# Performance work log

Measured on AMD Instinct MI355X. Metric: run time of the kernel, lower is better.

Reference implementation:

```python
import jax, jax.numpy as jnp
import numpy as np

NUP, NDOWN = 15, 15
NELEC = NUP + NDOWN
NATOMS = 10
NDIM = 3
NBATCH = 512
FEAT = 64   # hidden feature dim
K_RBF = 64  # gaussian RBF expansion size
NLAYERS = 2
RBF_CUT = 8.0


def _build_graphs():
    # elec-elec: upper-tri pairs, each pair -> 2 directed edges (i->j, j->i),
    # matching ree.repeat_interleave(2) edge-distance ordering.
    ii, jj = np.triu_indices(NELEC, k=1)                      # [435]
    ee_src = np.stack([ii, jj], 1).reshape(-1).astype(np.int32)  # [870]
    ee_dst = np.stack([jj, ii], 1).reshape(-1).astype(np.int32)
    ee_types = np.array([0] * NUP + [1] * NDOWN, np.int32)
    # elec-nuc: nodes = [electrons(0..29), atoms(30..39)];
    # ren is transposed to [natoms, nelec] then flattened -> atom-major pair order.
    aa = np.repeat(np.arange(NATOMS), NELEC)
    ee_ = np.tile(np.arange(NELEC), NATOMS)
    en_src = np.stack([ee_, NELEC + aa], 1).reshape(-1).astype(np.int32)  # [600]
    en_dst = np.stack([NELEC + aa, ee_], 1).reshape(-1).astype(np.int32)
    en_types = np.concatenate([np.array([0] * NUP + [1] * NDOWN),
                               2 + np.arange(NATOMS)]).astype(np.int32)
    return ee_src, ee_dst, ee_types, en_src, en_dst, en_types


def setup_inputs() -> dict:
    key = jax.random.key(0)
    ks = jax.random.split(key, 20)
    ee_src, ee_dst, ee_types, en_src, en_dst, en_types = _build_graphs()
    s = 0.1
    inp = {
        "pos": jax.random.normal(ks[0], (NBATCH, NELEC * NDIM), jnp.float32) * 2.0,
        "atoms": jax.random.normal(ks[1], (NATOMS, NDIM), jnp.float32) * 3.0,
        "emb_ee": jax.random.normal(ks[2], (2, FEAT), jnp.float32) * s,
        "wf_ee": jax.random.normal(ks[3], (K_RBF, FEAT), jnp.float32) * s,
        "bf_ee": jnp.zeros((FEAT,), jnp.float32),
        "wl_ee": jax.random.normal(ks[4], (NLAYERS, FEAT, FEAT), jnp.float32) * s,
        "bl_ee": jnp.zeros((NLAYERS, FEAT), jnp.float32),
        "wr_ee": jax.random.normal(ks[5], (FEAT, 1), jnp.float32) * s,
        "br_ee": jnp.zeros((1,), jnp.float32),
        "emb_en": jax.random.normal(ks[6], (2 + NATOMS, FEAT), jnp.float32) * s,
        "wf_en": jax.random.normal(ks[7], (K_RBF, FEAT), jnp.float32) * s,
        "bf_en": jnp.zeros((FEAT,), jnp.float32),
        "wl_en": jax.random.normal(ks[8], (NLAYERS, FEAT, FEAT), jnp.float32) * s,
        "bl_en": jnp.zeros((NLAYERS, FEAT), jnp.float32),
        "wr_en": jax.random.normal(ks[9], (FEAT, 1), jnp.float32) * s,
        "br_en": jnp.zeros((1,), jnp.float32),
        "ee_src": jnp.asarray(ee_src), "ee_dst": jnp.asarray(ee_dst),
        "ee_types": jnp.asarray(ee_types),
        "en_src": jnp.asarray(en_src), "en_dst": jnp.asarray(en_dst),
        "en_types": jnp.asarray(en_types),
    }
    return inp


def _gnn_kernel(types, src, dst, edist, emb, wf, bf, wl, bl, wr, br):
    """MGCN-style interaction net on a batch of identical graphs.
    types [N] int, src/dst [E] int, edist [nb, E] float."""
    nb = edist.shape[0]
    N = types.shape[0]
    centers = jnp.linspace(0.0, RBF_CUT, K_RBF).astype(edist.dtype)
    rbf = jnp.exp(-(edist[..., None] - centers) ** 2)        # [nb, E, K]
    filt = jnp.tanh(rbf @ wf + bf)                           # [nb, E, F]
    h = jnp.broadcast_to(emb[types][None], (nb, N, emb.shape[1]))  # [nb, N, F]
    for l in range(wl.shape[0]):
        m = h[:, src, :] * filt                              # gather + edge filter
        agg = jnp.zeros_like(h).at[:, dst, :].add(m)         # scatter-add messages
        h = h + jnp.tanh(agg @ wl[l] + bl[l])
    return h.sum(axis=1) @ wr + br                           # [nb, 1] readout


def reference(pos, atoms, emb_ee, wf_ee, bf_ee, wl_ee, bl_ee, wr_ee, br_ee,
              emb_en, wf_en, bf_en, wl_en, bl_en, wr_en, br_en,
              ee_src, ee_dst, ee_types, en_src, en_dst, en_types):
    nb = pos.shape[0]
    xyz = pos.reshape(nb, NELEC, NDIM)
    # elec-elec edge distances (src/dst index electron nodes; symmetric so this
    # equals extract_tri_up(...).repeat_interleave(2))
    d_ee = jnp.linalg.norm(xyz[:, ee_src] - xyz[:, ee_dst], axis=-1)   # [nb, 870]
    # elec-nuc: node positions = [electrons; atoms]
    nodepos = jnp.concatenate(
        [xyz, jnp.broadcast_to(atoms[None], (nb, NATOMS, NDIM))], axis=1)
    d_en = jnp.linalg.norm(nodepos[:, en_src] - nodepos[:, en_dst], axis=-1)  # [nb, 600]
    ee_k = _gnn_kernel(ee_types, ee_src, ee_dst, d_ee,
                       emb_ee, wf_ee, bf_ee, wl_ee, bl_ee, wr_ee, br_ee)
    en_k = _gnn_kernel(en_types, en_src, en_dst, d_en,
                       emb_en, wf_en, bf_en, wl_en, bl_en, wr_en, br_en)
    return jnp.exp(ee_k + en_k)   # [nb, 1] Jastrow factor (derivative=0)
```

## Files before the change

kernel.cpp:

```cpp
#include <hip/hip_runtime.h>
#include <math.h>

#define NB      512
#define NELEC   30
#define NATOMS  10
#define NNEN    40
#define FEAT    64
#define KRBF    64
#define BLOCK   1024
#define NWAVES  (BLOCK/64)
#define NPEE    435
#define NPEN    300
#define TILE    32
#define FPAD    65

#define OFF_XYZ    0
#define OFF_AXYZ   96
#define OFF_KEE    128
#define OFF_BASE   132
#define HS_OFF     OFF_BASE
#define AGG_OFF    (HS_OFF + NNEN*FEAT)
#define FILT_OFF   (AGG_OFF + NNEN*FEAT)
#define SM_TOTAL   (FILT_OFF + NPEE*FPAD)

__device__ __forceinline__ int ee_base(int i) { return 29*i - ((i*(i-1))>>1); }

__global__ __launch_bounds__(BLOCK)
void fused_kernel(const float* __restrict__ pos,
                  const float* __restrict__ atoms,
                  const float* __restrict__ emb_ee,
                  const float* __restrict__ wf_ee,
                  const float* __restrict__ bf_ee,
                  const float* __restrict__ wl_ee,
                  const float* __restrict__ bl_ee,
                  const float* __restrict__ wr_ee,
                  const float* __restrict__ br_ee,
                  const float* __restrict__ emb_en,
                  const float* __restrict__ wf_en,
                  const float* __restrict__ bf_en,
                  const float* __restrict__ wl_en,
                  const float* __restrict__ bl_en,
                  const float* __restrict__ wr_en,
                  const float* __restrict__ br_en,
                  const int*   __restrict__ ee_ty,
                  const int*   __restrict__ en_ty,
                  float*       __restrict__ out)
{
    extern __shared__ float sm[];
    float*  xyz  = sm + OFF_XYZ;
    float*  axyz = sm + OFF_AXYZ;
    double* keeP = reinterpret_cast<double*>(sm + OFF_KEE);
    float*  hS   = sm + HS_OFF;
    float*  aggS = sm + AGG_OFF;
    float*  filt = sm + FILT_OFF;

    const int tid  = threadIdx.x;
    const int b    = blockIdx.x;
    const int lane = tid & 63;
    const int w    = tid >> 6;
    const int q    = tid & 511;
    const int uoff = __builtin_amdgcn_readfirstlane((tid >> 9) * TILE);

    for (int idx = tid; idx < NELEC*3; idx += BLOCK) xyz[idx] = pos[b*NELEC*3 + idx];
    for (int idx = tid; idx < NATOMS*3; idx += BLOCK) axyz[idx] = atoms[idx];
    for (int idx = tid; idx < NELEC*FEAT; idx += BLOCK) {
        int n = idx >> 6, f = idx & 63;
        hS[idx] = emb_ee[ee_ty[n]*FEAT + f];
    }
    __syncthreads();

    {
        const int p = (q < NPEE) ? q : (NPEE - 1);
        {
            int i = 0, rem = p;
            while (rem >= NELEC - 1 - i) { rem -= NELEC - 1 - i; ++i; }
            const int j = i + 1 + rem;
            const float dx = xyz[3*i+0] - xyz[3*j+0];
            const float dy = xyz[3*i+1] - xyz[3*j+1];
            const float dz = xyz[3*i+2] - xyz[3*j+2];
            const float dd = sqrtf(dx*dx + dy*dy + dz*dz);

            float facc[TILE];
            const float* bfH = bf_ee + uoff;
            #pragma unroll
            for (int f = 0; f < TILE; ++f) facc[f] = bfH[f];
            #pragma unroll 2
            for (int k = 0; k < KRBF; ++k) {
                const float ck = (float)((double)k * (8.0/63.0));
                const float t  = dd - ck;
                const float rk = expf(-t*t);
                const float* wrow = wf_ee + k*FEAT + uoff;
                #pragma unroll
                for (int f = 0; f < TILE; ++f) facc[f] = fmaf(rk, wrow[f], facc[f]);
            }
            #pragma unroll
            for (int ff = 0; ff < TILE; ++ff)
                filt[p*FPAD + uoff + ff] = tanhf(facc[ff]);
        }
        __syncthreads();

        #pragma unroll
        for (int l = 0; l < 2; ++l) {
            const float* wlL = wl_ee + l*FEAT*FEAT;
            const float* blL = bl_ee + l*FEAT;

            #pragma unroll
            for (int pass = 0; pass < 2; ++pass) {
                const int idx = tid + pass*BLOCK;
                if (idx < NELEC*FEAT) {
                    const int i = idx >> 6;
                    const int f = idx & 63;
                    float a = 0.f;
                    #pragma unroll
                    for (int j = 0; j < NELEC; ++j) {
                        if (j != i) {
                            int pp = (j < i) ? (ee_base(j) + (i - j - 1))
                                             : (ee_base(i) + (j - i - 1));
                            a = fmaf(hS[j*FEAT + f], filt[pp*FPAD + f], a);
                        }
                    }
                    aggS[i*FEAT + f] = a;
                }
            }
            __syncthreads();

            for (int i = w; i < NELEC; i += NWAVES) {
                float a2 = 0.f;
                const float4* arow = reinterpret_cast<const float4*>(aggS + i*FEAT);
                #pragma unroll
                for (int k = 0; k < FEAT/4; ++k) {
                    float4 av = arow[k];
                    a2 = fmaf(av.x, wlL[(4*k+0)*FEAT + lane], a2);
                    a2 = fmaf(av.y, wlL[(4*k+1)*FEAT + lane], a2);
                    a2 = fmaf(av.z, wlL[(4*k+2)*FEAT + lane], a2);
                    a2 = fmaf(av.w, wlL[(4*k+3)*FEAT + lane], a2);
                }
                hS[i*FEAT + lane] += tanhf(a2 + blL[lane]);
            }
            __syncthreads();
        }

        if (w == 0) {
            float s = 0.f;
            #pragma unroll
            for (int n = 0; n < NELEC; ++n) s += hS[n*FEAT + lane];
            double dv = (double)s * (double)wr_ee[lane];
            #pragma unroll
            for (int o = 32; o > 0; o >>= 1) dv += __shfl_xor(dv, o, 64);
            if (lane == 0) *keeP = dv + (double)br_ee[0];
        }
    }
    __syncthreads();

    {
        for (int idx = tid; idx < NNEN*FEAT; idx += BLOCK) {
            int n = idx >> 6, f = idx & 63;
            hS[idx] = emb_en[en_ty[n]*FEAT + f];
        }

        const int p = (q < NPEN) ? q : (NPEN - 1);
        {
            const int a = p / NELEC;
            const int e = p - a*NELEC;
            const float dx = xyz[3*e+0] - axyz[3*a+0];
            const float dy = xyz[3*e+1] - axyz[3*a+1];
            const float dz = xyz[3*e+2] - axyz[3*a+2];
            const float dd = sqrtf(dx*dx + dy*dy + dz*dz);

            float facc[TILE];
            const float* bfH = bf_en + uoff;
            #pragma unroll
            for (int f = 0; f < TILE; ++f) facc[f] = bfH[f];
            #pragma unroll 2
            for (int k = 0; k < KRBF; ++k) {
                const float ck = (float)((double)k * (8.0/63.0));
                const float t  = dd - ck;
                const float rk = expf(-t*t);
                const float* wrow = wf_en + k*FEAT + uoff;
                #pragma unroll
                for (int f = 0; f < TILE; ++f) facc[f] = fmaf(rk, wrow[f], facc[f]);
            }
            #pragma unroll
            for (int ff = 0; ff < TILE; ++ff)
                filt[p*FPAD + uoff + ff] = tanhf(facc[ff]);
        }
        __syncthreads();

        #pragma unroll
        for (int l = 0; l < 2; ++l) {
            const float* wlL = wl_en + l*FEAT*FEAT;
            const float* blL = bl_en + l*FEAT;

            #pragma unroll
            for (int pass = 0; pass < 3; ++pass) {
                const int idx = tid + pass*BLOCK;
                if (idx < NNEN*FEAT) {
                    const int n = idx >> 6;
                    const int f = idx & 63;
                    float a = 0.f;
                    if (n < NELEC) {
                        #pragma unroll
                        for (int at = 0; at < NATOMS; ++at)
                            a = fmaf(hS[(NELEC+at)*FEAT + f],
                                     filt[(at*NELEC + n)*FPAD + f], a);
                    } else {
                        const int at = n - NELEC;
                        #pragma unroll
                        for (int e2 = 0; e2 < NELEC; ++e2)
                            a = fmaf(hS[e2*FEAT + f],
                                     filt[(at*NELEC + e2)*FPAD + f], a);
                    }
                    aggS[n*FEAT + f] = a;
                }
            }
            __syncthreads();

            for (int n = w; n < NNEN; n += NWAVES) {
                float a2 = 0.f;
                const float4* arow = reinterpret_cast<const float4*>(aggS + n*FEAT);
                #pragma unroll
                for (int k = 0; k < FEAT/4; ++k) {
                    float4 av = arow[k];
                    a2 = fmaf(av.x, wlL[(4*k+0)*FEAT + lane], a2);
                    a2 = fmaf(av.y, wlL[(4*k+1)*FEAT + lane], a2);
                    a2 = fmaf(av.z, wlL[(4*k+2)*FEAT + lane], a2);
                    a2 = fmaf(av.w, wlL[(4*k+3)*FEAT + lane], a2);
                }
                hS[n*FEAT + lane] += tanhf(a2 + blL[lane]);
            }
            __syncthreads();
        }

        if (w == 0) {
            float s = 0.f;
            #pragma unroll
            for (int n = 0; n < NNEN; ++n) s += hS[n*FEAT + lane];
            double dv = (double)s * (double)wr_en[lane];
            #pragma unroll
            for (int o = 32; o > 0; o >>= 1) dv += __shfl_xor(dv, o, 64);
            if (lane == 0) out[b] = (float)exp(dv + (double)br_en[0] + *keeP);
        }
    }
}

extern "C" void kernel_launch(void* const* d_in, const int* in_sizes, int n_in,
                              void* d_out, int out_size, void* d_ws, size_t ws_size,
                              hipStream_t stream) {
    const float* pos    = (const float*)d_in[0];
    const float* atoms  = (const float*)d_in[1];
    const float* emb_ee = (const float*)d_in[2];
    const float* wf_ee  = (const float*)d_in[3];
    const float* bf_ee  = (const float*)d_in[4];
    const float* wl_ee  = (const float*)d_in[5];
    const float* bl_ee  = (const float*)d_in[6];
    const float* wr_ee  = (const float*)d_in[7];
    const float* br_ee  = (const float*)d_in[8];
    const float* emb_en = (const float*)d_in[9];
    const float* wf_en  = (const float*)d_in[10];
    const float* bf_en  = (const float*)d_in[11];
    const float* wl_en  = (const float*)d_in[12];
    const float* bl_en  = (const float*)d_in[13];
    const float* wr_en  = (const float*)d_in[14];
    const float* br_en  = (const float*)d_in[15];
    const int*   ee_ty  = (const int*)d_in[18];
    const int*   en_ty  = (const int*)d_in[21];

    float* out = (float*)d_out;

    (void)hipFuncSetAttribute((const void*)fused_kernel,
            hipFuncAttributeMaxDynamicSharedMemorySize, SM_TOTAL*(int)sizeof(float));

    fused_kernel<<<NB, BLOCK, SM_TOTAL*sizeof(float), stream>>>(
        pos, atoms,
        emb_ee, wf_ee, bf_ee, wl_ee, bl_ee, wr_ee, br_ee,
        emb_en, wf_en, bf_en, wl_en, bl_en, wr_en, br_en,
        ee_ty, en_ty, out);
}
```

Before: 221.5 us.

## Fuse aggregation and linear per wave with ping-pong node buffers, fewer barriers

The message aggregation and the dense layer are merged into one per-wave pass. Each wave computes the aggregated row for one node into a private scratch row in shared memory, then applies the weight matrix directly. Node features now alternate between two buffers, so one barrier per layer disappears and the in-place update is gone. The ee readout is overlapped with the en filter computation, and the en filter is split across specific waves with inactive padded threads skipped. The catch is that only 30-40 nodes are processed by 16 waves, so per-layer parallelism drops from one thread per (node, feature) to one wave per node.

```diff
diff --git a/kernel.cpp b/kernel.cpp
--- a/kernel.cpp
+++ b/kernel.cpp
@@ -13,17 +13,109 @@
 #define NPEN    300
 #define TILE    32
 #define FPAD    65
+#define WROW    64
 
 #define OFF_XYZ    0
 #define OFF_AXYZ   96
 #define OFF_KEE    128
-#define OFF_BASE   132
-#define HS_OFF     OFF_BASE
-#define AGG_OFF    (HS_OFF + NNEN*FEAT)
-#define FILT_OFF   (AGG_OFF + NNEN*FEAT)
+#define H0_OFF     132
+#define H1_OFF     (H0_OFF + NNEN*FEAT)
+#define WR_OFF     (H1_OFF + NNEN*FEAT)
+#define FILT_OFF   (WR_OFF + NWAVES*WROW)
 #define SM_TOTAL   (FILT_OFF + NPEE*FPAD)
 
 __device__ __forceinline__ int ee_base(int i) { return 29*i - ((i*(i-1))>>1); }
+
+__device__ __forceinline__ void ee_layer(const float* __restrict__ hc,
+                                         float* __restrict__ hn,
+                                         const float* __restrict__ filt,
+                                         float* __restrict__ wr,
+                                         const float* __restrict__ wlL,
+                                         const float* __restrict__ blL,
+                                         int w, int lane)
+{
+    for (int i = w; i < NELEC; i += NWAVES) {
+        float a = 0.f;
+        #pragma unroll
+        for (int j = 0; j < NELEC; ++j) {
+            if (j != i) {
+                int pp = (j < i) ? (ee_base(j) + (i - j - 1))
+                                 : (ee_base(i) + (j - i - 1));
+                a = fmaf(hc[j*FEAT + lane], filt[pp*FPAD + lane], a);
+            }
+        }
+        wr[lane] = a;
+        float a2 = 0.f;
+        const float4* arow = reinterpret_cast<const float4*>(wr);
+        #pragma unroll
+        for (int k = 0; k < FEAT/4; ++k) {
+            float4 av = arow[k];
+            a2 = fmaf(av.x, wlL[(4*k+0)*FEAT + lane], a2);
+            a2 = fmaf(av.y, wlL[(4*k+1)*FEAT + lane], a2);
+            a2 = fmaf(av.z, wlL[(4*k+2)*FEAT + lane], a2);
+            a2 = fmaf(av.w, wlL[(4*k+3)*FEAT + lane], a2);
+        }
+        hn[i*FEAT + lane] = hc[i*FEAT + lane] + tanhf(a2 + blL[lane]);
+    }
+}
+
+__device__ __forceinline__ void en_layer(const float* __restrict__ hc,
+                                         float* __restrict__ hn,
+                                         const float* __restrict__ filt,
+                                         float* __restrict__ wr,
+                                         const float* __restrict__ wlL,
+                                         const float* __restrict__ blL,
+                                         int w, int lane)
+{
+    for (int n = w; n < NNEN; n += NWAVES) {
+        float a = 0.f;
+        if (n < NELEC) {
+            #pragma unroll
+            for (int at = 0; at < NATOMS; ++at)
+                a = fmaf(hc[(NELEC+at)*FEAT + lane],
+                         filt[(at*NELEC + n)*FPAD + lane], a);
+        } else {
+            const int at = n - NELEC;
+            #pragma unroll
+            for (int e2 = 0; e2 < NELEC; ++e2)
+                a = fmaf(hc[e2*FEAT + lane],
+                         filt[(at*NELEC + e2)*FPAD + lane], a);
+        }
+        wr[lane] = a;
+        float a2 = 0.f;
+        const float4* arow = reinterpret_cast<const float4*>(wr);
+        #pragma unroll
+        for (int k = 0; k < FEAT/4; ++k) {
+            float4 av = arow[k];
+            a2 = fmaf(av.x, wlL[(4*k+0)*FEAT + lane], a2);
+            a2 = fmaf(av.y, wlL[(4*k+1)*FEAT + lane], a2);
+            a2 = fmaf(av.z, wlL[(4*k+2)*FEAT + lane], a2);
+            a2 = fmaf(av.w, wlL[(4*k+3)*FEAT + lane], a2);
+        }
+        hn[n*FEAT + lane] = hc[n*FEAT + lane] + tanhf(a2 + blL[lane]);
+    }
+}
+
+__device__ __forceinline__ void rbf_filter(float dd, const float* __restrict__ wf,
+                                           const float* __restrict__ bf,
+                                           int uoff, float* __restrict__ dstrow)
+{
+    float facc[TILE];
+    const float* bfH = bf + uoff;
+    #pragma unroll
+    for (int f = 0; f < TILE; ++f) facc[f] = bfH[f];
+    #pragma unroll 2
+    for (int k = 0; k < KRBF; ++k) {
+        const float ck = (float)((double)k * (8.0/63.0));
+        const float t  = dd - ck;
+        const float rk = expf(-t*t);
+        const float* wrow = wf + k*FEAT + uoff;
+        #pragma unroll
+        for (int f = 0; f < TILE; ++f) facc[f] = fmaf(rk, wrow[f], facc[f]);
+    }
+    #pragma unroll
+    for (int ff = 0; ff < TILE; ++ff) dstrow[uoff + ff] = tanhf(facc[ff]);
+}
 
 __global__ __launch_bounds__(BLOCK)
 void fused_kernel(const float* __restrict__ pos,
@@ -50,8 +142,9 @@
     float*  xyz  = sm + OFF_XYZ;
     float*  axyz = sm + OFF_AXYZ;
     double* keeP = reinterpret_cast<double*>(sm + OFF_KEE);
-    float*  hS   = sm + HS_OFF;
-    float*  aggS = sm + AGG_OFF;
+    float*  h0   = sm + H0_OFF;
+    float*  h1   = sm + H1_OFF;
+    float*  wrS  = sm + WR_OFF;
     float*  filt = sm + FILT_OFF;
 
     const int tid  = threadIdx.x;
@@ -60,186 +153,80 @@
     const int w    = tid >> 6;
     const int q    = tid & 511;
     const int uoff = __builtin_amdgcn_readfirstlane((tid >> 9) * TILE);
+    float* wr = wrS + w*WROW;
 
     for (int idx = tid; idx < NELEC*3; idx += BLOCK) xyz[idx] = pos[b*NELEC*3 + idx];
     for (int idx = tid; idx < NATOMS*3; idx += BLOCK) axyz[idx] = atoms[idx];
     for (int idx = tid; idx < NELEC*FEAT; idx += BLOCK) {
         int n = idx >> 6, f = idx & 63;
-        hS[idx] = emb_ee[ee_ty[n]*FEAT + f];
-    }
-    __syncthreads();
-
+        h0[idx] = emb_ee[ee_ty[n]*FEAT + f];
+    }
+    __syncthreads();
+
+    if (q < NPEE) {
+        const int p = q;
+        int i = 0, rem = p;
+        while (rem >= NELEC - 1 - i) { rem -= NELEC - 1 - i; ++i; }
+        const int j = i + 1 + rem;
+        const float dx = xyz[3*i+0] - xyz[3*j+0];
+        const float dy = xyz[3*i+1] - xyz[3*j+1];
+        const float dz = xyz[3*i+2] - xyz[3*j+2];
+        const float dd = sqrtf(dx*dx + dy*dy + dz*dz);
+        rbf_filter(dd, wf_ee, bf_ee, uoff, filt + p*FPAD);
+    }
+    __syncthreads();
+
+    ee_layer(h0, h1, filt, wr, wl_ee + 0*FEAT*FEAT, bl_ee + 0*FEAT, w, lane);
+    __syncthreads();
+    ee_layer(h1, h0, filt, wr, wl_ee + 1*FEAT*FEAT, bl_ee + 1*FEAT, w, lane);
+    __syncthreads();
+
+    for (int idx = tid; idx < NNEN*FEAT; idx += BLOCK) {
+        int n = idx >> 6, f = idx & 63;
+        h1[idx] = emb_en[en_ty[n]*FEAT + f];
+    }
     {
-        const int p = (q < NPEE) ? q : (NPEE - 1);
-        {
-            int i = 0, rem = p;
-            while (rem >= NELEC - 1 - i) { rem -= NELEC - 1 - i; ++i; }
-            const int j = i + 1 + rem;
-            const float dx = xyz[3*i+0] - xyz[3*j+0];
-            const float dy = xyz[3*i+1] - xyz[3*j+1];
-            const float dz = xyz[3*i+2] - xyz[3*j+2];
-            const float dd = sqrtf(dx*dx + dy*dy + dz*dz);
-
-            float facc[TILE];
-            const float* bfH = bf_ee + uoff;
-            #pragma unroll
-            for (int f = 0; f < TILE; ++f) facc[f] = bfH[f];
-            #pragma unroll 2
-            for (int k = 0; k < KRBF; ++k) {
-                const float ck = (float)((double)k * (8.0/63.0));
-                const float t  = dd - ck;
-                const float rk = expf(-t*t);
-                const float* wrow = wf_ee + k*FEAT + uoff;
-                #pragma unroll
-                for (int f = 0; f < TILE; ++f) facc[f] = fmaf(rk, wrow[f], facc[f]);
+        const int v = w & 7;
+        const int blk = (w < 8) ? (v < 5 ? v : -1)
+                                : ((v >= 1 && v <= 3) ? v - 1
+                                   : (v == 5 || v == 6) ? v - 2 : -1);
+        if (blk >= 0) {
+            const int p = blk*64 + lane;
+            if (p < NPEN) {
+                const int a = p / NELEC;
+                const int e = p - a*NELEC;
+                const float dx = xyz[3*e+0] - axyz[3*a+0];
+                const float dy = xyz[3*e+1] - axyz[3*a+1];
+                const float dz = xyz[3*e+2] - axyz[3*a+2];
+                const float dd = sqrtf(dx*dx + dy*dy + dz*dz);
+                rbf_filter(dd, wf_en, bf_en, uoff, filt + p*FPAD);
             }
-            #pragma unroll
-            for (int ff = 0; ff < TILE; ++ff)
-                filt[p*FPAD + uoff + ff] = tanhf(facc[ff]);
-        }
-        __syncthreads();
-
-        #pragma unroll
-        for (int l = 0; l < 2; ++l) {
-            const float* wlL = wl_ee + l*FEAT*FEAT;
-            const float* blL = bl_ee + l*FEAT;
-
-            #pragma unroll
-            for (int pass = 0; pass < 2; ++pass) {
-                const int idx = tid + pass*BLOCK;
-                if (idx < NELEC*FEAT) {
-                    const int i = idx >> 6;
-                    const int f = idx & 63;
-                    float a = 0.f;
-                    #pragma unroll
-                    for (int j = 0; j < NELEC; ++j) {
-                        if (j != i) {
-                            int pp = (j < i) ? (ee_base(j) + (i - j - 1))
-                                             : (ee_base(i) + (j - i - 1));
-                            a = fmaf(hS[j*FEAT + f], filt[pp*FPAD + f], a);
-                        }
-                    }
-                    aggS[i*FEAT + f] = a;
-                }
-            }
-            __syncthreads();
-
-            for (int i = w; i < NELEC; i += NWAVES) {
-                float a2 = 0.f;
-                const float4* arow = reinterpret_cast<const float4*>(aggS + i*FEAT);
-                #pragma unroll
-                for (int k = 0; k < FEAT/4; ++k) {
-                    float4 av = arow[k];
-                    a2 = fmaf(av.x, wlL[(4*k+0)*FEAT + lane], a2);
-                    a2 = fmaf(av.y, wlL[(4*k+1)*FEAT + lane], a2);
-                    a2 = fmaf(av.z, wlL[(4*k+2)*FEAT + lane], a2);
-                    a2 = fmaf(av.w, wlL[(4*k+3)*FEAT + lane], a2);
-                }
-                hS[i*FEAT + lane] += tanhf(a2 + blL[lane]);
-            }
-            __syncthreads();
-        }
-
-        if (w == 0) {
-            float s = 0.f;
-            #pragma unroll
-            for (int n = 0; n < NELEC; ++n) s += hS[n*FEAT + lane];
-            double dv = (double)s * (double)wr_ee[lane];
-            #pragma unroll
-            for (int o = 32; o > 0; o >>= 1) dv += __shfl_xor(dv, o, 64);
-            if (lane == 0) *keeP = dv + (double)br_ee[0];
-        }
-    }
-    __syncthreads();
-
-    {
-        for (int idx = tid; idx < NNEN*FEAT; idx += BLOCK) {
-            int n = idx >> 6, f = idx & 63;
-            hS[idx] = emb_en[en_ty[n]*FEAT + f];
-        }
-
-        const int p = (q < NPEN) ? q : (NPEN - 1);
-        {
-            const int a = p / NELEC;
-            const int e = p - a*NELEC;
-            const float dx = xyz[3*e+0] - axyz[3*a+0];
-            const float dy = xyz[3*e+1] - axyz[3*a+1];
-            const float dz = xyz[3*e+2] - axyz[3*a+2];
-            const float dd = sqrtf(dx*dx + dy*dy + dz*dz);
-
-            float facc[TILE];
-            const float* bfH = bf_en + uoff;
-            #pragma unroll
-            for (int f = 0; f < TILE; ++f) facc[f] = bfH[f];
-            #pragma unroll 2
-            for (int k = 0; k < KRBF; ++k) {
-                const float ck = (float)((double)k * (8.0/63.0));
-                const float t  = dd - ck;
-                const float rk = expf(-t*t);
-                const float* wrow = wf_en + k*FEAT + uoff;
-                #pragma unroll
-                for (int f = 0; f < TILE; ++f) facc[f] = fmaf(rk, wrow[f], facc[f]);
-            }
-            #pragma unroll
-            for (int ff = 0; ff < TILE; ++ff)
-                filt[p*FPAD + uoff + ff] = tanhf(facc[ff]);
-        }
-        __syncthreads();
-
-        #pragma unroll
-        for (int l = 0; l < 2; ++l) {
-            const float* wlL = wl_en + l*FEAT*FEAT;
-            const float* blL = bl_en + l*FEAT;
-
-            #pragma unroll
-            for (int pass = 0; pass < 3; ++pass) {
-                const int idx = tid + pass*BLOCK;
-                if (idx < NNEN*FEAT) {
-                    const int n = idx >> 6;
-                    const int f = idx & 63;
-                    float a = 0.f;
-                    if (n < NELEC) {
-                        #pragma unroll
-                        for (int at = 0; at < NATOMS; ++at)
-                            a = fmaf(hS[(NELEC+at)*FEAT + f],
-                                     filt[(at*NELEC + n)*FPAD + f], a);
-                    } else {
-                        const int at = n - NELEC;
-                        #pragma unroll
-                        for (int e2 = 0; e2 < NELEC; ++e2)
-                            a = fmaf(hS[e2*FEAT + f],
-                                     filt[(at*NELEC + e2)*FPAD + f], a);
-                    }
-                    aggS[n*FEAT + f] = a;
-                }
-            }
-            __syncthreads();
-
-            for (int n = w; n < NNEN; n += NWAVES) {
-                float a2 = 0.f;
-                const float4* arow = reinterpret_cast<const float4*>(aggS + n*FEAT);
-                #pragma unroll
-                for (int k = 0; k < FEAT/4; ++k) {
-                    float4 av = arow[k];
-                    a2 = fmaf(av.x, wlL[(4*k+0)*FEAT + lane], a2);
-                    a2 = fmaf(av.y, wlL[(4*k+1)*FEAT + lane], a2);
-                    a2 = fmaf(av.z, wlL[(4*k+2)*FEAT + lane], a2);
-                    a2 = fmaf(av.w, wlL[(4*k+3)*FEAT + lane], a2);
-                }
-                hS[n*FEAT + lane] += tanhf(a2 + blL[lane]);
-            }
-            __syncthreads();
-        }
-
-        if (w == 0) {
-            float s = 0.f;
-            #pragma unroll
-            for (int n = 0; n < NNEN; ++n) s += hS[n*FEAT + lane];
-            double dv = (double)s * (double)wr_en[lane];
-            #pragma unroll
-            for (int o = 32; o > 0; o >>= 1) dv += __shfl_xor(dv, o, 64);
-            if (lane == 0) out[b] = (float)exp(dv + (double)br_en[0] + *keeP);
-        }
+        }
+    }
+    if (w == 0) {
+        float s = 0.f;
+        #pragma unroll
+        for (int n = 0; n < NELEC; ++n) s += h0[n*FEAT + lane];
+        double dv = (double)s * (double)wr_ee[lane];
+        #pragma unroll
+        for (int o = 32; o > 0; o >>= 1) dv += __shfl_xor(dv, o, 64);
+        if (lane == 0) *keeP = dv + (double)br_ee[0];
+    }
+    __syncthreads();
+
+    en_layer(h1, h0, filt, wr, wl_en + 0*FEAT*FEAT, bl_en + 0*FEAT, w, lane);
+    __syncthreads();
+    en_layer(h0, h1, filt, wr, wl_en + 1*FEAT*FEAT, bl_en + 1*FEAT, w, lane);
+    __syncthreads();
+
+    if (w == 0) {
+        float s = 0.f;
+        #pragma unroll
+        for (int n = 0; n < NNEN; ++n) s += h1[n*FEAT + lane];
+        double dv = (double)s * (double)wr_en[lane];
+        #pragma unroll
+        for (int o = 32; o > 0; o >>= 1) dv += __shfl_xor(dv, o, 64);
+        if (lane == 0) out[b] = (float)exp(dv + (double)br_en[0] + *keeP);
     }
 }
 
```

New measurement: 215.8 us. 1.03x faster.

## Keep RBF filter halves in registers and stage them through a half-width LDS buffer

Applied to the files above, without the earlier changes.

Each thread now computes a full pair's filter for one 32-feature half and keeps the tanh outputs in registers. Only one half at a time is written to a 33-float-padded shared buffer, and the aggregation runs in two half passes with the second half written between them. This shrinks shared memory by about half, which may allow more blocks per CU. It also skips the clamped duplicate pair work and swaps the h/agg buffers in the electron-nuclear stage to overlap embedding init with filter compute. The cost is extra barriers, re-writing the filter each layer, and high register pressure from the live facc array.

```diff
diff --git a/kernel.cpp b/kernel.cpp
--- a/kernel.cpp
+++ b/kernel.cpp
@@ -12,18 +12,65 @@
 #define NPEE    435
 #define NPEN    300
 #define TILE    32
-#define FPAD    65
-
-#define OFF_XYZ    0
-#define OFF_AXYZ   96
-#define OFF_KEE    128
-#define OFF_BASE   132
-#define HS_OFF     OFF_BASE
-#define AGG_OFF    (HS_OFF + NNEN*FEAT)
-#define FILT_OFF   (AGG_OFF + NNEN*FEAT)
-#define SM_TOTAL   (FILT_OFF + NPEE*FPAD)
+#define FPAD    33
+
+#define OFF_XYZ   0
+#define OFF_AXYZ  96
+#define OFF_KEE   128
+#define HS_OFF    132
+#define AGG_OFF   (HS_OFF + NNEN*FEAT)
+#define FT_OFF    (AGG_OFF + NNEN*FEAT)
+#define SM_TOTAL  (FT_OFF + NPEE*FPAD)
 
 __device__ __forceinline__ int ee_base(int i) { return 29*i - ((i*(i-1))>>1); }
+
+__device__ __forceinline__ void rbf_filter(float dd, const float* __restrict__ wf,
+                                           const float* __restrict__ bf,
+                                           int uoff, float* __restrict__ facc)
+{
+    const float* bfH = bf + uoff;
+    #pragma unroll
+    for (int f = 0; f < TILE; ++f) facc[f] = bfH[f];
+    #pragma unroll 2
+    for (int k = 0; k < KRBF; ++k) {
+        const float ck = (float)((double)k * (8.0/63.0));
+        const float t  = dd - ck;
+        const float rk = expf(-t*t);
+        const float* wrow = wf + k*FEAT + uoff;
+        #pragma unroll
+        for (int f = 0; f < TILE; ++f) facc[f] = fmaf(rk, wrow[f], facc[f]);
+    }
+    #pragma unroll
+    for (int f = 0; f < TILE; ++f) facc[f] = tanhf(facc[f]);
+}
+
+__device__ __forceinline__ void ft_write(const float* __restrict__ facc,
+                                         float* __restrict__ fT, int p)
+{
+    #pragma unroll
+    for (int ff = 0; ff < TILE; ++ff) fT[p*FPAD + ff] = facc[ff];
+}
+
+__device__ __forceinline__ void dense_update(const float* __restrict__ aggbuf,
+                                             float* __restrict__ hbuf,
+                                             const float* __restrict__ wlL,
+                                             const float* __restrict__ blL,
+                                             int N, int w, int lane)
+{
+    for (int i = w; i < N; i += NWAVES) {
+        float a2 = 0.f;
+        const float4* arow = reinterpret_cast<const float4*>(aggbuf + i*FEAT);
+        #pragma unroll
+        for (int k = 0; k < FEAT/4; ++k) {
+            float4 av = arow[k];
+            a2 = fmaf(av.x, wlL[(4*k+0)*FEAT + lane], a2);
+            a2 = fmaf(av.y, wlL[(4*k+1)*FEAT + lane], a2);
+            a2 = fmaf(av.z, wlL[(4*k+2)*FEAT + lane], a2);
+            a2 = fmaf(av.w, wlL[(4*k+3)*FEAT + lane], a2);
+        }
+        hbuf[i*FEAT + lane] += tanhf(a2 + blL[lane]);
+    }
+}
 
 __global__ __launch_bounds__(BLOCK)
 void fused_kernel(const float* __restrict__ pos,
@@ -52,14 +99,30 @@
     double* keeP = reinterpret_cast<double*>(sm + OFF_KEE);
     float*  hS   = sm + HS_OFF;
     float*  aggS = sm + AGG_OFF;
-    float*  filt = sm + FILT_OFF;
+    float*  fT   = sm + FT_OFF;
 
     const int tid  = threadIdx.x;
     const int b    = blockIdx.x;
     const int lane = tid & 63;
     const int w    = tid >> 6;
-    const int q    = tid & 511;
-    const int uoff = __builtin_amdgcn_readfirstlane((tid >> 9) * TILE);
+
+    const int  ee_t   = (w >= 7) ? 1 : 0;
+    const int  ee_p   = ((w >= 7 ? w - 7 : w) << 6) | lane;
+    const bool ee_ok  = (w < 14) && (ee_p < NPEE);
+    const int  v      = w & 7;
+    const int  en_blk = (w < 8) ? (v < 5 ? v : -1)
+                                : ((v >= 1 && v <= 3) ? v - 1
+                                   : (v == 5 || v == 6) ? v - 2 : -1);
+    const int  en_t   = (w >= 8) ? 1 : 0;
+    const int  en_p   = (en_blk < 0) ? 0 : ((en_blk << 6) | lane);
+    const bool en_ok  = (en_blk >= 0) && (en_p < NPEN);
+    const int  hr     = (w == 5) ? 0 : (w == 6) ? 1 : (w == 7) ? 2
+                      : (w == 8) ? 3 : (w == 12) ? 4 : -1;
+
+    const int uoff_ee = __builtin_amdgcn_readfirstlane(ee_t * TILE);
+    const int uoff_en = __builtin_amdgcn_readfirstlane(en_t * TILE);
+
+    float facc[TILE];
 
     for (int idx = tid; idx < NELEC*3; idx += BLOCK) xyz[idx] = pos[b*NELEC*3 + idx];
     for (int idx = tid; idx < NATOMS*3; idx += BLOCK) axyz[idx] = atoms[idx];
@@ -69,177 +132,129 @@
     }
     __syncthreads();
 
-    {
-        const int p = (q < NPEE) ? q : (NPEE - 1);
-        {
-            int i = 0, rem = p;
-            while (rem >= NELEC - 1 - i) { rem -= NELEC - 1 - i; ++i; }
-            const int j = i + 1 + rem;
-            const float dx = xyz[3*i+0] - xyz[3*j+0];
-            const float dy = xyz[3*i+1] - xyz[3*j+1];
-            const float dz = xyz[3*i+2] - xyz[3*j+2];
-            const float dd = sqrtf(dx*dx + dy*dy + dz*dz);
-
-            float facc[TILE];
-            const float* bfH = bf_ee + uoff;
-            #pragma unroll
-            for (int f = 0; f < TILE; ++f) facc[f] = bfH[f];
-            #pragma unroll 2
-            for (int k = 0; k < KRBF; ++k) {
-                const float ck = (float)((double)k * (8.0/63.0));
-                const float t  = dd - ck;
-                const float rk = expf(-t*t);
-                const float* wrow = wf_ee + k*FEAT + uoff;
+    if (ee_ok) {
+        int i = 0, rem = ee_p;
+        while (rem >= NELEC - 1 - i) { rem -= NELEC - 1 - i; ++i; }
+        const int j = i + 1 + rem;
+        const float dx = xyz[3*i+0] - xyz[3*j+0];
+        const float dy = xyz[3*i+1] - xyz[3*j+1];
+        const float dz = xyz[3*i+2] - xyz[3*j+2];
+        const float dd = sqrtf(dx*dx + dy*dy + dz*dz);
+        rbf_filter(dd, wf_ee, bf_ee, uoff_ee, facc);
+        if (ee_t == 0) ft_write(facc, fT, ee_p);
+    }
+    __syncthreads();
+
+    #pragma unroll
+    for (int l = 0; l < 2; ++l) {
+        const float* wlL = wl_ee + l*FEAT*FEAT;
+        const float* blL = bl_ee + l*FEAT;
+
+        #pragma unroll
+        for (int t = 0; t < 2; ++t) {
+            if (t == 1) {
+                if (ee_ok && ee_t == 1) ft_write(facc, fT, ee_p);
+                __syncthreads();
+            }
+            if (tid < NELEC*TILE) {
+                const int i  = tid >> 5;
+                const int ff = tid & 31;
+                const int f  = t*TILE + ff;
+                float a = 0.f;
                 #pragma unroll
-                for (int f = 0; f < TILE; ++f) facc[f] = fmaf(rk, wrow[f], facc[f]);
-            }
-            #pragma unroll
-            for (int ff = 0; ff < TILE; ++ff)
-                filt[p*FPAD + uoff + ff] = tanhf(facc[ff]);
-        }
+                for (int j = 0; j < NELEC; ++j) {
+                    if (j != i) {
+                        int pp = (j < i) ? (ee_base(j) + (i - j - 1))
+                                         : (ee_base(i) + (j - i - 1));
+                        a = fmaf(hS[j*FEAT + f], fT[pp*FPAD + ff], a);
+                    }
+                }
+                aggS[i*FEAT + f] = a;
+            }
+            __syncthreads();
+        }
+        dense_update(aggS, hS, wlL, blL, NELEC, w, lane);
+        if (l == 0 && ee_ok && ee_t == 0) ft_write(facc, fT, ee_p);
         __syncthreads();
-
-        #pragma unroll
-        for (int l = 0; l < 2; ++l) {
-            const float* wlL = wl_ee + l*FEAT*FEAT;
-            const float* blL = bl_ee + l*FEAT;
-
+    }
+
+    if (w == 15) {
+        float s = 0.f;
+        #pragma unroll
+        for (int n = 0; n < NELEC; ++n) s += hS[n*FEAT + lane];
+        double dv = (double)s * (double)wr_ee[lane];
+        #pragma unroll
+        for (int o = 32; o > 0; o >>= 1) dv += __shfl_xor(dv, o, 64);
+        if (lane == 0) *keeP = dv + (double)br_ee[0];
+    }
+    if (hr >= 0) {
+        #pragma unroll
+        for (int r = 0; r < 8; ++r) {
+            const int idx = hr*64 + lane + r*320;
+            aggS[idx] = emb_en[en_ty[idx >> 6]*FEAT + (idx & 63)];
+        }
+    }
+    if (en_ok) {
+        const int a = en_p / NELEC;
+        const int e = en_p - a*NELEC;
+        const float dx = xyz[3*e+0] - axyz[3*a+0];
+        const float dy = xyz[3*e+1] - axyz[3*a+1];
+        const float dz = xyz[3*e+2] - axyz[3*a+2];
+        const float dd = sqrtf(dx*dx + dy*dy + dz*dz);
+        rbf_filter(dd, wf_en, bf_en, uoff_en, facc);
+        if (en_t == 0) ft_write(facc, fT, en_p);
+    }
+    __syncthreads();
+
+    #pragma unroll
+    for (int l = 0; l < 2; ++l) {
+        const float* wlL = wl_en + l*FEAT*FEAT;
+        const float* blL = bl_en + l*FEAT;
+
+        #pragma unroll
+        for (int t = 0; t < 2; ++t) {
+            if (t == 1) {
+                if (en_ok && en_t == 1) ft_write(facc, fT, en_p);
+                __syncthreads();
+            }
             #pragma unroll
             for (int pass = 0; pass < 2; ++pass) {
                 const int idx = tid + pass*BLOCK;
-                if (idx < NELEC*FEAT) {
-                    const int i = idx >> 6;
-                    const int f = idx & 63;
-                    float a = 0.f;
-                    #pragma unroll
-                    for (int j = 0; j < NELEC; ++j) {
-                        if (j != i) {
-                            int pp = (j < i) ? (ee_base(j) + (i - j - 1))
-                                             : (ee_base(i) + (j - i - 1));
-                            a = fmaf(hS[j*FEAT + f], filt[pp*FPAD + f], a);
-                        }
-                    }
-                    aggS[i*FEAT + f] = a;
-                }
-            }
-            __syncthreads();
-
-            for (int i = w; i < NELEC; i += NWAVES) {
-                float a2 = 0.f;
-                const float4* arow = reinterpret_cast<const float4*>(aggS + i*FEAT);
-                #pragma unroll
-                for (int k = 0; k < FEAT/4; ++k) {
-                    float4 av = arow[k];
-                    a2 = fmaf(av.x, wlL[(4*k+0)*FEAT + lane], a2);
-                    a2 = fmaf(av.y, wlL[(4*k+1)*FEAT + lane], a2);
-                    a2 = fmaf(av.z, wlL[(4*k+2)*FEAT + lane], a2);
-                    a2 = fmaf(av.w, wlL[(4*k+3)*FEAT + lane], a2);
-                }
-                hS[i*FEAT + lane] += tanhf(a2 + blL[lane]);
-            }
-            __syncthreads();
-        }
-
-        if (w == 0) {
-            float s = 0.f;
-            #pragma unroll
-            for (int n = 0; n < NELEC; ++n) s += hS[n*FEAT + lane];
-            double dv = (double)s * (double)wr_ee[lane];
-            #pragma unroll
-            for (int o = 32; o > 0; o >>= 1) dv += __shfl_xor(dv, o, 64);
-            if (lane == 0) *keeP = dv + (double)br_ee[0];
-        }
-    }
-    __syncthreads();
-
-    {
-        for (int idx = tid; idx < NNEN*FEAT; idx += BLOCK) {
-            int n = idx >> 6, f = idx & 63;
-            hS[idx] = emb_en[en_ty[n]*FEAT + f];
-        }
-
-        const int p = (q < NPEN) ? q : (NPEN - 1);
-        {
-            const int a = p / NELEC;
-            const int e = p - a*NELEC;
-            const float dx = xyz[3*e+0] - axyz[3*a+0];
-            const float dy = xyz[3*e+1] - axyz[3*a+1];
-            const float dz = xyz[3*e+2] - axyz[3*a+2];
-            const float dd = sqrtf(dx*dx + dy*dy + dz*dz);
-
-            float facc[TILE];
-            const float* bfH = bf_en + uoff;
-            #pragma unroll
-            for (int f = 0; f < TILE; ++f) facc[f] = bfH[f];
-            #pragma unroll 2
-            for (int k = 0; k < KRBF; ++k) {
-                const float ck = (float)((double)k * (8.0/63.0));
-                const float t  = dd - ck;
-                const float rk = expf(-t*t);
-                const float* wrow = wf_en + k*FEAT + uoff;
-                #pragma unroll
-                for (int f = 0; f < TILE; ++f) facc[f] = fmaf(rk, wrow[f], facc[f]);
-            }
-            #pragma unroll
-            for (int ff = 0; ff < TILE; ++ff)
-                filt[p*FPAD + uoff + ff] = tanhf(facc[ff]);
-        }
-        __syncthreads();
-
-        #pragma unroll
-        for (int l = 0; l < 2; ++l) {
-            const float* wlL = wl_en + l*FEAT*FEAT;
-            const float* blL = bl_en + l*FEAT;
-
-            #pragma unroll
-            for (int pass = 0; pass < 3; ++pass) {
-                const int idx = tid + pass*BLOCK;
-                if (idx < NNEN*FEAT) {
-                    const int n = idx >> 6;
-                    const int f = idx & 63;
+                if (idx < NNEN*TILE) {
+                    const int n  = idx >> 5;
+                    const int ff = idx & 31;
+                    const int f  = t*TILE + ff;
                     float a = 0.f;
                     if (n < NELEC) {
                         #pragma unroll
                         for (int at = 0; at < NATOMS; ++at)
-                            a = fmaf(hS[(NELEC+at)*FEAT + f],
-                                     filt[(at*NELEC + n)*FPAD + f], a);
+                            a = fmaf(aggS[(NELEC+at)*FEAT + f],
+                                     fT[(at*NELEC + n)*FPAD + ff], a);
                     } else {
                         const int at = n - NELEC;
                         #pragma unroll
                         for (int e2 = 0; e2 < NELEC; ++e2)
-                            a = fmaf(hS[e2*FEAT + f],
-                                     filt[(at*NELEC + e2)*FPAD + f], a);
+                            a = fmaf(aggS[e2*FEAT + f],
+                                     fT[(at*NELEC + e2)*FPAD + ff], a);
                     }
-                    aggS[n*FEAT + f] = a;
+                    hS[n*FEAT + f] = a;
                 }
             }
             __syncthreads();
-
-            for (int n = w; n < NNEN; n += NWAVES) {
-                float a2 = 0.f;
-                const float4* arow = reinterpret_cast<const float4*>(aggS + n*FEAT);
-                #pragma unroll
-                for (int k = 0; k < FEAT/4; ++k) {
-                    float4 av = arow[k];
-                    a2 = fmaf(av.x, wlL[(4*k+0)*FEAT + lane], a2);
-                    a2 = fmaf(av.y, wlL[(4*k+1)*FEAT + lane], a2);
-                    a2 = fmaf(av.z, wlL[(4*k+2)*FEAT + lane], a2);
-                    a2 = fmaf(av.w, wlL[(4*k+3)*FEAT + lane], a2);
-                }
-                hS[n*FEAT + lane] += tanhf(a2 + blL[lane]);
-            }
-            __syncthreads();
-        }
-
-        if (w == 0) {
-            float s = 0.f;
-            #pragma unroll
-            for (int n = 0; n < NNEN; ++n) s += hS[n*FEAT + lane];
-            double dv = (double)s * (double)wr_en[lane];
-            #pragma unroll
-            for (int o = 32; o > 0; o >>= 1) dv += __shfl_xor(dv, o, 64);
-            if (lane == 0) out[b] = (float)exp(dv + (double)br_en[0] + *keeP);
-        }
+        }
+        dense_update(hS, aggS, wlL, blL, NNEN, w, lane);
+        if (l == 0 && en_ok && en_t == 0) ft_write(facc, fT, en_p);
+        __syncthreads();
+    }
+
+    if (w == 0) {
+        float s = 0.f;
+        #pragma unroll
+        for (int n = 0; n < NNEN; ++n) s += aggS[n*FEAT + lane];
+        double dv = (double)s * (double)wr_en[lane];
+        #pragma unroll
+        for (int o = 32; o > 0; o >>= 1) dv += __shfl_xor(dv, o, 64);
+        if (lane == 0) out[b] = (float)exp(dv + (double)br_en[0] + *keeP);
     }
 }
 
```

After: 655.3 us. 2.96x slower.
